# Performance work log

Measured on AMD Instinct MI355X. Metric: run time of the kernel, lower is better.

Reference implementation:

```python
import jax, jax.numpy as jnp
import numpy as np

T, H, I = 8192, 2048, 768  # tokens, hidden_size, intermediate_size

def setup_inputs() -> dict:
    key = jax.random.key(0)
    k1, k2, k3, k4 = jax.random.split(key, 4)
    x = jax.random.normal(k1, (T, H), dtype=jnp.float32)
    # torch nn.Linear weight layout: [out_features, in_features]
    gate_w = jax.random.normal(k2, (I, H), dtype=jnp.float32) * (1.0 / np.sqrt(H))
    up_w = jax.random.normal(k3, (I, H), dtype=jnp.float32) * (1.0 / np.sqrt(H))
    down_w = jax.random.normal(k4, (H, I), dtype=jnp.float32) * (1.0 / np.sqrt(I))
    return {"x": x, "gate_w": gate_w, "up_w": up_w, "down_w": down_w}

def reference(x, gate_w, up_w, down_w):
    # fused SwiGLU MLP: down( silu(x @ gate^T) * (x @ up^T) )
    gate = jnp.einsum('th,ih->ti', x, gate_w)   # [T, I]
    up = jnp.einsum('th,ih->ti', x, up_w)       # [T, I]
    h = jax.nn.silu(gate) * up                   # [T, I]
    out = jnp.einsum('ti,hi->th', h, down_w)     # [T, H]
    return out
```

## Files before the change

### kernel.cpp

```cpp
#include <hip/hip_runtime.h>
#include <hip/hip_bf16.h>
#include <stdint.h>

#define T_DIM 8192
#define H_DIM 2048
#define I_DIM 768

typedef __bf16 bf16_t;
typedef bf16_t bf16x8 __attribute__((ext_vector_type(8)));
typedef bf16_t bf16x4 __attribute__((ext_vector_type(4)));
typedef float  f32x4  __attribute__((ext_vector_type(4)));

__device__ __forceinline__ void async_load16(const void* g, void* s) {
    __builtin_amdgcn_global_load_lds(
        (const __attribute__((address_space(1))) void*)g,
        (__attribute__((address_space(3))) void*)s, 16, 0, 0);
}

__global__ __launch_bounds__(256) void cvt_kernel(
    const float* __restrict__ X, const float* __restrict__ G,
    const float* __restrict__ U, const float* __restrict__ D,
    bf16_t* __restrict__ Xb, bf16_t* __restrict__ Gb,
    bf16_t* __restrict__ Ub, bf16_t* __restrict__ Db)
{
    const size_t N8X = (size_t)T_DIM * H_DIM / 8;
    const size_t N8W = (size_t)I_DIM * H_DIM / 8;
    const size_t total = N8X + 3 * N8W;
    for (size_t i = (size_t)blockIdx.x * blockDim.x + threadIdx.x; i < total;
         i += (size_t)gridDim.x * blockDim.x) {
        const float* s; bf16_t* d; size_t j = i;
        if (j < N8X) { s = X; d = Xb; }
        else {
            j -= N8X;
            if (j < N8W) { s = G; d = Gb; }
            else { j -= N8W;
                if (j < N8W) { s = U; d = Ub; }
                else { j -= N8W; s = D; d = Db; } }
        }
        float4 v0 = ((const float4*)s)[2 * j];
        float4 v1 = ((const float4*)s)[2 * j + 1];
        bf16x8 o;
        o[0] = (bf16_t)v0.x; o[1] = (bf16_t)v0.y; o[2] = (bf16_t)v0.z; o[3] = (bf16_t)v0.w;
        o[4] = (bf16_t)v1.x; o[5] = (bf16_t)v1.y; o[6] = (bf16_t)v1.z; o[7] = (bf16_t)v1.w;
        ((bf16x8*)d)[j] = o;
    }
}

__global__ __launch_bounds__(256) void gateup_kernel(
    const bf16_t* __restrict__ X,
    const bf16_t* __restrict__ Wg,
    const bf16_t* __restrict__ Wu,
    bf16_t* __restrict__ Hbuf)
{
    __shared__ __align__(16) bf16_t sA[128 * 32];
    __shared__ __align__(16) bf16_t sG[64 * 32];
    __shared__ __align__(16) bf16_t sU[64 * 32];

    const int tid   = threadIdx.x;
    const int lane  = tid & 63;
    const int wave  = tid >> 6;
    const int waveM = wave >> 1;
    const int waveN = wave & 1;
    const int quad  = lane >> 4;
    const int lrow  = lane & 15;

    const int blockM = blockIdx.x;
    const int blockN = blockIdx.y;

    f32x4 accG[4][2], accU[4][2];
#pragma unroll
    for (int i = 0; i < 4; i++)
#pragma unroll
        for (int j = 0; j < 2; j++) { accG[i][j] = (f32x4)(0.f); accU[i][j] = (f32x4)(0.f); }

    const int s0 = tid, s1 = tid + 256;
    const int rA0 = s0 >> 2, cA0 = (s0 & 3) * 8;
    const int rA1 = s1 >> 2, cA1 = (s1 & 3) * 8;
    const int rW  = tid >> 2, cW  = (tid & 3) * 8;

    const bf16_t* Ab = X  + (size_t)(blockM * 128) * H_DIM;
    const bf16_t* Gb = Wg + (size_t)(blockN * 64) * H_DIM;
    const bf16_t* Ub = Wu + (size_t)(blockN * 64) * H_DIM;

    for (int k0 = 0; k0 < H_DIM; k0 += 32) {
        async_load16(Ab + (size_t)rA0 * H_DIM + k0 + cA0, &sA[s0 * 8]);
        async_load16(Ab + (size_t)rA1 * H_DIM + k0 + cA1, &sA[s1 * 8]);
        async_load16(Gb + (size_t)rW  * H_DIM + k0 + cW,  &sG[tid * 8]);
        async_load16(Ub + (size_t)rW  * H_DIM + k0 + cW,  &sU[tid * 8]);
        __syncthreads();

        bf16x8 aF[4], gF[2], uF[2];
#pragma unroll
        for (int mi = 0; mi < 4; mi++) {
            int r = waveM * 64 + mi * 16 + lrow;
            aF[mi] = *(const bf16x8*)&sA[r * 32 + quad * 8];
        }
#pragma unroll
        for (int ni = 0; ni < 2; ni++) {
            int r = waveN * 32 + ni * 16 + lrow;
            gF[ni] = *(const bf16x8*)&sG[r * 32 + quad * 8];
            uF[ni] = *(const bf16x8*)&sU[r * 32 + quad * 8];
        }
        __syncthreads();

#pragma unroll
        for (int mi = 0; mi < 4; mi++)
#pragma unroll
            for (int ni = 0; ni < 2; ni++) {
                accG[mi][ni] = __builtin_amdgcn_mfma_f32_16x16x32_bf16(aF[mi], gF[ni], accG[mi][ni], 0, 0, 0);
                accU[mi][ni] = __builtin_amdgcn_mfma_f32_16x16x32_bf16(aF[mi], uF[ni], accU[mi][ni], 0, 0, 0);
            }
    }

#pragma unroll
    for (int mi = 0; mi < 4; mi++) {
#pragma unroll
        for (int ni = 0; ni < 2; ni++) {
#pragma unroll
            for (int r = 0; r < 4; r++) {
                int row = blockM * 128 + waveM * 64 + mi * 16 + quad * 4 + r;
                int col = blockN * 64 + waveN * 32 + ni * 16 + lrow;
                float g = accG[mi][ni][r];
                float u = accU[mi][ni][r];
                float h = (g / (1.f + __expf(-g))) * u;
                Hbuf[(size_t)row * I_DIM + col] = (bf16_t)h;
            }
        }
    }
}

__global__ __launch_bounds__(256, 4) void down_kernel(
    const bf16_t* __restrict__ Hbuf,
    const bf16_t* __restrict__ Wd,
    float* __restrict__ Out)
{
    __shared__ __align__(16) bf16_t sA[128 * 64];
    __shared__ __align__(16) bf16_t sB[128 * 64];

    const int tid   = threadIdx.x;
    const int lane  = tid & 63;
    const int wave  = tid >> 6;
    const int waveM = wave >> 1;
    const int waveN = wave & 1;
    const int quad  = lane >> 4;
    const int lrow  = lane & 15;

    const int blockM = blockIdx.x;
    const int blockN = blockIdx.y;

    f32x4 acc[4][4];
#pragma unroll
    for (int i = 0; i < 4; i++)
#pragma unroll
        for (int j = 0; j < 4; j++) acc[i][j] = (f32x4)(0.f);

    const bf16_t* Ab = Hbuf + (size_t)(blockM * 128) * I_DIM;
    const bf16_t* Bb = Wd   + (size_t)(blockN * 128) * I_DIM;

    int gRow[4], gCol[4];
#pragma unroll
    for (int i = 0; i < 4; i++) {
        int s = tid + 256 * i;
        gRow[i] = s >> 3;
        gCol[i] = ((s & 7) ^ ((s >> 3) & 7)) * 8;
    }

    int aOff[4], bOff[4];
#pragma unroll
    for (int mi = 0; mi < 4; mi++) {
        int r = waveM * 64 + mi * 16 + lrow;
        aOff[mi] = r * 64 + ((quad ^ (r & 7)) * 8);
    }
#pragma unroll
    for (int ni = 0; ni < 4; ni++) {
        int r = waveN * 64 + ni * 16 + lrow;
        bOff[ni] = r * 64 + ((quad ^ (r & 7)) * 8);
    }

    for (int k0 = 0; k0 < I_DIM; k0 += 64) {
#pragma unroll
        for (int i = 0; i < 4; i++) {
            async_load16(Ab + (size_t)gRow[i] * I_DIM + k0 + gCol[i],
                         &sA[(tid + 256 * i) * 8]);
            async_load16(Bb + (size_t)gRow[i] * I_DIM + k0 + gCol[i],
                         &sB[(tid + 256 * i) * 8]);
        }
        __syncthreads();

#pragma unroll
        for (int kk = 0; kk < 2; kk++) {
            const int kx = kk * 32;
            bf16x8 aF[4], bF[4];
#pragma unroll
            for (int mi = 0; mi < 4; mi++)
                aF[mi] = *(const bf16x8*)&sA[aOff[mi] ^ kx];
#pragma unroll
            for (int ni = 0; ni < 4; ni++)
                bF[ni] = *(const bf16x8*)&sB[bOff[ni] ^ kx];
#pragma unroll
            for (int mi = 0; mi < 4; mi++)
#pragma unroll
                for (int ni = 0; ni < 4; ni++)
                    acc[mi][ni] = __builtin_amdgcn_mfma_f32_16x16x32_bf16(aF[mi], bF[ni], acc[mi][ni], 0, 0, 0);
        }
        __syncthreads();
    }

#pragma unroll
    for (int mi = 0; mi < 4; mi++) {
#pragma unroll
        for (int ni = 0; ni < 4; ni++) {
#pragma unroll
            for (int r = 0; r < 4; r++) {
                int row = blockM * 128 + waveM * 64 + mi * 16 + quad * 4 + r;
                int col = blockN * 128 + waveN * 64 + ni * 16 + lrow;
                Out[(size_t)row * H_DIM + col] = acc[mi][ni][r];
            }
        }
    }
}

extern "C" void kernel_launch(void* const* d_in, const int* in_sizes, int n_in,
                              void* d_out, int out_size, void* d_ws, size_t ws_size,
                              hipStream_t stream) {
    const float* x  = (const float*)d_in[0];
    const float* gw = (const float*)d_in[1];
    const float* uw = (const float*)d_in[2];
    const float* dw = (const float*)d_in[3];
    float* out = (float*)d_out;

    bf16_t* xb = (bf16_t*)d_ws;
    bf16_t* gb = xb + (size_t)T_DIM * H_DIM;
    bf16_t* ub = gb + (size_t)I_DIM * H_DIM;
    bf16_t* db = ub + (size_t)I_DIM * H_DIM;
    bf16_t* hb = db + (size_t)I_DIM * H_DIM;

    cvt_kernel<<<2048, 256, 0, stream>>>(x, gw, uw, dw, xb, gb, ub, db);
    gateup_kernel<<<dim3(T_DIM / 128, I_DIM / 64), 256, 0, stream>>>(xb, gb, ub, hb);
    down_kernel<<<dim3(T_DIM / 128, H_DIM / 128), 256, 0, stream>>>(hb, db, out);
}
```

Before: 223.2 us.

## Use 512-thread blocks in gate/up kernel with XOR-swizzled LDS tiles

The gate/up GEMM kernel now runs 8 waves per block instead of 4. Each wave computes a 64x16 slice instead of 64x32, so per-thread accumulators shrink and more waves can hide latency. The LDS fill is spread so each thread issues two async loads, and the LDS layout is XOR-swizzled to cut bank conflicts on fragment reads. The cost is lower MFMA work per wave relative to LDS reads, plus more barrier participants per iteration.

```diff
diff --git a/kernel.cpp b/kernel.cpp
--- a/kernel.cpp
+++ b/kernel.cpp
@@ -46,7 +46,7 @@
     }
 }
 
-__global__ __launch_bounds__(256) void gateup_kernel(
+__global__ __launch_bounds__(512, 8) void gateup_kernel(
     const bf16_t* __restrict__ X,
     const bf16_t* __restrict__ Wg,
     const bf16_t* __restrict__ Wu,
@@ -59,72 +59,66 @@
     const int tid   = threadIdx.x;
     const int lane  = tid & 63;
     const int wave  = tid >> 6;
-    const int waveM = wave >> 1;
-    const int waveN = wave & 1;
+    const int waveM = wave >> 2;
+    const int waveN = wave & 3;
     const int quad  = lane >> 4;
     const int lrow  = lane & 15;
 
     const int blockM = blockIdx.x;
     const int blockN = blockIdx.y;
 
-    f32x4 accG[4][2], accU[4][2];
-#pragma unroll
-    for (int i = 0; i < 4; i++)
-#pragma unroll
-        for (int j = 0; j < 2; j++) { accG[i][j] = (f32x4)(0.f); accU[i][j] = (f32x4)(0.f); }
-
-    const int s0 = tid, s1 = tid + 256;
-    const int rA0 = s0 >> 2, cA0 = (s0 & 3) * 8;
-    const int rA1 = s1 >> 2, cA1 = (s1 & 3) * 8;
-    const int rW  = tid >> 2, cW  = (tid & 3) * 8;
+    f32x4 accG[4], accU[4];
+#pragma unroll
+    for (int i = 0; i < 4; i++) { accG[i] = (f32x4)(0.f); accU[i] = (f32x4)(0.f); }
+
+    const int sa = tid;
+    const int rA = sa >> 2, cA = (((sa & 3) ^ ((rA >> 1) & 3)) * 8);
+    const int sw = tid & 255;
+    const int rW = sw >> 2, cW = (((sw & 3) ^ ((rW >> 1) & 3)) * 8);
 
     const bf16_t* Ab = X  + (size_t)(blockM * 128) * H_DIM;
-    const bf16_t* Gb = Wg + (size_t)(blockN * 64) * H_DIM;
-    const bf16_t* Ub = Wu + (size_t)(blockN * 64) * H_DIM;
+    const bf16_t* Wb = ((tid < 256) ? Wg : Wu) + (size_t)(blockN * 64) * H_DIM;
+    bf16_t* sW = (tid < 256) ? &sG[sw * 8] : &sU[sw * 8];
+
+    int aOff[4];
+#pragma unroll
+    for (int mi = 0; mi < 4; mi++) {
+        int r = waveM * 64 + mi * 16 + lrow;
+        aOff[mi] = r * 32 + ((quad ^ ((r >> 1) & 3)) * 8);
+    }
+    const int rw = waveN * 16 + lrow;
+    const int wOff = rw * 32 + ((quad ^ ((rw >> 1) & 3)) * 8);
 
     for (int k0 = 0; k0 < H_DIM; k0 += 32) {
-        async_load16(Ab + (size_t)rA0 * H_DIM + k0 + cA0, &sA[s0 * 8]);
-        async_load16(Ab + (size_t)rA1 * H_DIM + k0 + cA1, &sA[s1 * 8]);
-        async_load16(Gb + (size_t)rW  * H_DIM + k0 + cW,  &sG[tid * 8]);
-        async_load16(Ub + (size_t)rW  * H_DIM + k0 + cW,  &sU[tid * 8]);
-        __syncthreads();
-
-        bf16x8 aF[4], gF[2], uF[2];
+        async_load16(Ab + (size_t)rA * H_DIM + k0 + cA, &sA[sa * 8]);
+        async_load16(Wb + (size_t)rW * H_DIM + k0 + cW, sW);
+        __syncthreads();
+
+        bf16x8 aF[4], gF, uF;
+#pragma unroll
+        for (int mi = 0; mi < 4; mi++)
+            aF[mi] = *(const bf16x8*)&sA[aOff[mi]];
+        gF = *(const bf16x8*)&sG[wOff];
+        uF = *(const bf16x8*)&sU[wOff];
+        __syncthreads();
+
 #pragma unroll
         for (int mi = 0; mi < 4; mi++) {
-            int r = waveM * 64 + mi * 16 + lrow;
-            aF[mi] = *(const bf16x8*)&sA[r * 32 + quad * 8];
-        }
-#pragma unroll
-        for (int ni = 0; ni < 2; ni++) {
-            int r = waveN * 32 + ni * 16 + lrow;
-            gF[ni] = *(const bf16x8*)&sG[r * 32 + quad * 8];
-            uF[ni] = *(const bf16x8*)&sU[r * 32 + quad * 8];
-        }
-        __syncthreads();
-
-#pragma unroll
-        for (int mi = 0; mi < 4; mi++)
-#pragma unroll
-            for (int ni = 0; ni < 2; ni++) {
-                accG[mi][ni] = __builtin_amdgcn_mfma_f32_16x16x32_bf16(aF[mi], gF[ni], accG[mi][ni], 0, 0, 0);
-                accU[mi][ni] = __builtin_amdgcn_mfma_f32_16x16x32_bf16(aF[mi], uF[ni], accU[mi][ni], 0, 0, 0);
-            }
-    }
-
-#pragma unroll
-    for (int mi = 0; mi < 4; mi++) {
-#pragma unroll
-        for (int ni = 0; ni < 2; ni++) {
-#pragma unroll
-            for (int r = 0; r < 4; r++) {
-                int row = blockM * 128 + waveM * 64 + mi * 16 + quad * 4 + r;
-                int col = blockN * 64 + waveN * 32 + ni * 16 + lrow;
-                float g = accG[mi][ni][r];
-                float u = accU[mi][ni][r];
-                float h = (g / (1.f + __expf(-g))) * u;
-                Hbuf[(size_t)row * I_DIM + col] = (bf16_t)h;
-            }
+            accG[mi] = __builtin_amdgcn_mfma_f32_16x16x32_bf16(aF[mi], gF, accG[mi], 0, 0, 0);
+            accU[mi] = __builtin_amdgcn_mfma_f32_16x16x32_bf16(aF[mi], uF, accU[mi], 0, 0, 0);
+        }
+    }
+
+#pragma unroll
+    for (int mi = 0; mi < 4; mi++) {
+#pragma unroll
+        for (int r = 0; r < 4; r++) {
+            int row = blockM * 128 + waveM * 64 + mi * 16 + quad * 4 + r;
+            int col = blockN * 64 + waveN * 16 + lrow;
+            float g = accG[mi][r];
+            float u = accU[mi][r];
+            float h = (g / (1.f + __expf(-g))) * u;
+            Hbuf[(size_t)row * I_DIM + col] = (bf16_t)h;
         }
     }
 }
@@ -236,6 +230,6 @@
     bf16_t* hb = db + (size_t)I_DIM * H_DIM;
 
     cvt_kernel<<<2048, 256, 0, stream>>>(x, gw, uw, dw, xb, gb, ub, db);
-    gateup_kernel<<<dim3(T_DIM / 128, I_DIM / 64), 256, 0, stream>>>(xb, gb, ub, hb);
+    gateup_kernel<<<dim3(T_DIM / 128, I_DIM / 64), 512, 0, stream>>>(xb, gb, ub, hb);
     down_kernel<<<dim3(T_DIM / 128, H_DIM / 128), 256, 0, stream>>>(hb, db, out);
 }
```

Result: slower. 262.0 us (+17.4%).

## Fuse fp32-to-bf16 conversion of X and gate/up weights into gate-up GEMM

Applied to the files above, without the earlier changes.

Removes the separate conversion pass for X, gate and up weights. The gate/up kernel now loads fp32 tiles into registers, converts them to bf16 and stores them into XOR-swizzled LDS, with precomputed fragment offsets. Only the down weights are still pre-converted, in a smaller kernel. This saves a full write and re-read of the bf16 activation copy. In exchange, global reads are fp32 (twice the bytes for reused tiles) and the async global-to-LDS loads become synchronous register loads, which may expose latency.

```diff
diff --git a/kernel.cpp b/kernel.cpp
--- a/kernel.cpp
+++ b/kernel.cpp
@@ -17,39 +17,29 @@
         (__attribute__((address_space(3))) void*)s, 16, 0, 0);
 }
 
-__global__ __launch_bounds__(256) void cvt_kernel(
-    const float* __restrict__ X, const float* __restrict__ G,
-    const float* __restrict__ U, const float* __restrict__ D,
-    bf16_t* __restrict__ Xb, bf16_t* __restrict__ Gb,
-    bf16_t* __restrict__ Ub, bf16_t* __restrict__ Db)
+__device__ __forceinline__ bf16x8 cvt8(float4 a, float4 b) {
+    bf16x8 o;
+    o[0] = (bf16_t)a.x; o[1] = (bf16_t)a.y; o[2] = (bf16_t)a.z; o[3] = (bf16_t)a.w;
+    o[4] = (bf16_t)b.x; o[5] = (bf16_t)b.y; o[6] = (bf16_t)b.z; o[7] = (bf16_t)b.w;
+    return o;
+}
+
+__global__ __launch_bounds__(256) void cvt_d_kernel(
+    const float* __restrict__ D, bf16_t* __restrict__ Db)
 {
-    const size_t N8X = (size_t)T_DIM * H_DIM / 8;
-    const size_t N8W = (size_t)I_DIM * H_DIM / 8;
-    const size_t total = N8X + 3 * N8W;
-    for (size_t i = (size_t)blockIdx.x * blockDim.x + threadIdx.x; i < total;
-         i += (size_t)gridDim.x * blockDim.x) {
-        const float* s; bf16_t* d; size_t j = i;
-        if (j < N8X) { s = X; d = Xb; }
-        else {
-            j -= N8X;
-            if (j < N8W) { s = G; d = Gb; }
-            else { j -= N8W;
-                if (j < N8W) { s = U; d = Ub; }
-                else { j -= N8W; s = D; d = Db; } }
-        }
-        float4 v0 = ((const float4*)s)[2 * j];
-        float4 v1 = ((const float4*)s)[2 * j + 1];
-        bf16x8 o;
-        o[0] = (bf16_t)v0.x; o[1] = (bf16_t)v0.y; o[2] = (bf16_t)v0.z; o[3] = (bf16_t)v0.w;
-        o[4] = (bf16_t)v1.x; o[5] = (bf16_t)v1.y; o[6] = (bf16_t)v1.z; o[7] = (bf16_t)v1.w;
-        ((bf16x8*)d)[j] = o;
+    const size_t N8 = (size_t)I_DIM * H_DIM / 8;
+    for (size_t j = (size_t)blockIdx.x * blockDim.x + threadIdx.x; j < N8;
+         j += (size_t)gridDim.x * blockDim.x) {
+        float4 v0 = ((const float4*)D)[2 * j];
+        float4 v1 = ((const float4*)D)[2 * j + 1];
+        ((bf16x8*)Db)[j] = cvt8(v0, v1);
     }
 }
 
 __global__ __launch_bounds__(256) void gateup_kernel(
-    const bf16_t* __restrict__ X,
-    const bf16_t* __restrict__ Wg,
-    const bf16_t* __restrict__ Wu,
+    const float* __restrict__ Xf,
+    const float* __restrict__ Wgf,
+    const float* __restrict__ Wuf,
     bf16_t* __restrict__ Hbuf)
 {
     __shared__ __align__(16) bf16_t sA[128 * 32];
@@ -78,30 +68,55 @@
     const int rA1 = s1 >> 2, cA1 = (s1 & 3) * 8;
     const int rW  = tid >> 2, cW  = (tid & 3) * 8;
 
-    const bf16_t* Ab = X  + (size_t)(blockM * 128) * H_DIM;
-    const bf16_t* Gb = Wg + (size_t)(blockN * 64) * H_DIM;
-    const bf16_t* Ub = Wu + (size_t)(blockN * 64) * H_DIM;
+    const int dA0 = rA0 * 32 + (((s0 & 3) ^ ((rA0 >> 1) & 3)) * 8);
+    const int dA1 = rA1 * 32 + (((s1 & 3) ^ ((rA1 >> 1) & 3)) * 8);
+    const int dW  = rW  * 32 + (((tid & 3) ^ ((rW  >> 1) & 3)) * 8);
+
+    const float* Ab0 = Xf  + (size_t)(blockM * 128 + rA0) * H_DIM + cA0;
+    const float* Ab1 = Xf  + (size_t)(blockM * 128 + rA1) * H_DIM + cA1;
+    const float* Gb  = Wgf + (size_t)(blockN * 64  + rW ) * H_DIM + cW;
+    const float* Ub  = Wuf + (size_t)(blockN * 64  + rW ) * H_DIM + cW;
+
+    int aOff[4], wOff[2];
+#pragma unroll
+    for (int mi = 0; mi < 4; mi++) {
+        int r = waveM * 64 + mi * 16 + lrow;
+        aOff[mi] = r * 32 + ((quad ^ ((r >> 1) & 3)) * 8);
+    }
+#pragma unroll
+    for (int ni = 0; ni < 2; ni++) {
+        int r = waveN * 32 + ni * 16 + lrow;
+        wOff[ni] = r * 32 + ((quad ^ ((r >> 1) & 3)) * 8);
+    }
 
     for (int k0 = 0; k0 < H_DIM; k0 += 32) {
-        async_load16(Ab + (size_t)rA0 * H_DIM + k0 + cA0, &sA[s0 * 8]);
-        async_load16(Ab + (size_t)rA1 * H_DIM + k0 + cA1, &sA[s1 * 8]);
-        async_load16(Gb + (size_t)rW  * H_DIM + k0 + cW,  &sG[tid * 8]);
-        async_load16(Ub + (size_t)rW  * H_DIM + k0 + cW,  &sU[tid * 8]);
+        float4 a00 = ((const float4*)(Ab0 + k0))[0];
+        float4 a01 = ((const float4*)(Ab0 + k0))[1];
+        float4 a10 = ((const float4*)(Ab1 + k0))[0];
+        float4 a11 = ((const float4*)(Ab1 + k0))[1];
+        float4 g0  = ((const float4*)(Gb  + k0))[0];
+        float4 g1  = ((const float4*)(Gb  + k0))[1];
+        float4 u0  = ((const float4*)(Ub  + k0))[0];
+        float4 u1  = ((const float4*)(Ub  + k0))[1];
+
+        __syncthreads();
+
+        *(bf16x8*)&sA[dA0] = cvt8(a00, a01);
+        *(bf16x8*)&sA[dA1] = cvt8(a10, a11);
+        *(bf16x8*)&sG[dW]  = cvt8(g0, g1);
+        *(bf16x8*)&sU[dW]  = cvt8(u0, u1);
+
         __syncthreads();
 
         bf16x8 aF[4], gF[2], uF[2];
 #pragma unroll
-        for (int mi = 0; mi < 4; mi++) {
-            int r = waveM * 64 + mi * 16 + lrow;
-            aF[mi] = *(const bf16x8*)&sA[r * 32 + quad * 8];
-        }
+        for (int mi = 0; mi < 4; mi++)
+            aF[mi] = *(const bf16x8*)&sA[aOff[mi]];
 #pragma unroll
         for (int ni = 0; ni < 2; ni++) {
-            int r = waveN * 32 + ni * 16 + lrow;
-            gF[ni] = *(const bf16x8*)&sG[r * 32 + quad * 8];
-            uF[ni] = *(const bf16x8*)&sU[r * 32 + quad * 8];
-        }
-        __syncthreads();
+            gF[ni] = *(const bf16x8*)&sG[wOff[ni]];
+            uF[ni] = *(const bf16x8*)&sU[wOff[ni]];
+        }
 
 #pragma unroll
         for (int mi = 0; mi < 4; mi++)
@@ -229,13 +244,10 @@
     const float* dw = (const float*)d_in[3];
     float* out = (float*)d_out;
 
-    bf16_t* xb = (bf16_t*)d_ws;
-    bf16_t* gb = xb + (size_t)T_DIM * H_DIM;
-    bf16_t* ub = gb + (size_t)I_DIM * H_DIM;
-    bf16_t* db = ub + (size_t)I_DIM * H_DIM;
+    bf16_t* db = (bf16_t*)d_ws;
     bf16_t* hb = db + (size_t)I_DIM * H_DIM;
 
-    cvt_kernel<<<2048, 256, 0, stream>>>(x, gw, uw, dw, xb, gb, ub, db);
-    gateup_kernel<<<dim3(T_DIM / 128, I_DIM / 64), 256, 0, stream>>>(xb, gb, ub, hb);
+    cvt_d_kernel<<<512, 256, 0, stream>>>(dw, db);
+    gateup_kernel<<<dim3(T_DIM / 128, I_DIM / 64), 256, 0, stream>>>(x, gw, uw, hb);
     down_kernel<<<dim3(T_DIM / 128, H_DIM / 128), 256, 0, stream>>>(hb, db, out);
 }
```

New measurement: 236.4 us. 1.06x slower.

## Double-buffer down GEMM with 256x256 tiles and phased MFMA scheduling

Applied to the files above, without the earlier changes.

Rewrites the down-projection kernel to use 512-thread blocks computing 256x256 output tiles, with double-buffered LDS staging of H and the down weights. Async loads for the next K-tiles are issued between MFMA phases, with explicit waitcnt, barriers and priority hints, so that memory traffic overlaps compute. The larger tiles increase data reuse, but they use a large amount of LDS and give a grid of only 256 blocks, which limits occupancy and load balance.

```diff
diff --git a/kernel.cpp b/kernel.cpp
--- a/kernel.cpp
+++ b/kernel.cpp
@@ -15,6 +15,19 @@
     __builtin_amdgcn_global_load_lds(
         (const __attribute__((address_space(1))) void*)g,
         (__attribute__((address_space(3))) void*)s, 16, 0, 0);
+}
+
+__device__ __forceinline__ void phase_barrier() {
+    asm volatile("" ::: "memory");
+    __builtin_amdgcn_s_barrier();
+    asm volatile("" ::: "memory");
+}
+
+__device__ __forceinline__ bf16x8 cvt8(float4 a, float4 b) {
+    bf16x8 o;
+    o[0] = (bf16_t)a.x; o[1] = (bf16_t)a.y; o[2] = (bf16_t)a.z; o[3] = (bf16_t)a.w;
+    o[4] = (bf16_t)b.x; o[5] = (bf16_t)b.y; o[6] = (bf16_t)b.z; o[7] = (bf16_t)b.w;
+    return o;
 }
 
 __global__ __launch_bounds__(256) void cvt_kernel(
@@ -39,10 +52,7 @@
         }
         float4 v0 = ((const float4*)s)[2 * j];
         float4 v1 = ((const float4*)s)[2 * j + 1];
-        bf16x8 o;
-        o[0] = (bf16_t)v0.x; o[1] = (bf16_t)v0.y; o[2] = (bf16_t)v0.z; o[3] = (bf16_t)v0.w;
-        o[4] = (bf16_t)v1.x; o[5] = (bf16_t)v1.y; o[6] = (bf16_t)v1.z; o[7] = (bf16_t)v1.w;
-        ((bf16x8*)d)[j] = o;
+        ((bf16x8*)d)[j] = cvt8(v0, v1);
     }
 }
 
@@ -129,91 +139,126 @@
     }
 }
 
-__global__ __launch_bounds__(256, 4) void down_kernel(
+__global__ __launch_bounds__(512, 2) void down_kernel(
     const bf16_t* __restrict__ Hbuf,
     const bf16_t* __restrict__ Wd,
     float* __restrict__ Out)
 {
-    __shared__ __align__(16) bf16_t sA[128 * 64];
-    __shared__ __align__(16) bf16_t sB[128 * 64];
-
-    const int tid   = threadIdx.x;
-    const int lane  = tid & 63;
-    const int wave  = tid >> 6;
-    const int waveM = wave >> 1;
-    const int waveN = wave & 1;
-    const int quad  = lane >> 4;
-    const int lrow  = lane & 15;
-
-    const int blockM = blockIdx.x;
-    const int blockN = blockIdx.y;
-
-    f32x4 acc[4][4];
-#pragma unroll
-    for (int i = 0; i < 4; i++)
+    __shared__ __align__(16) bf16_t sA[2][256 * 64];
+    __shared__ __align__(16) bf16_t sB[2][256 * 64];
+
+    const int tid  = threadIdx.x;
+    const int lane = tid & 63;
+    const int wave = tid >> 6;
+    const int wm   = wave >> 2;
+    const int wn   = wave & 3;
+    const int quad = lane >> 4;
+    const int lrow = lane & 15;
+
+    const int bm = blockIdx.x;
+    const int bn = blockIdx.y;
+
+    f32x4 acc[8][4];
+#pragma unroll
+    for (int i = 0; i < 8; i++)
 #pragma unroll
         for (int j = 0; j < 4; j++) acc[i][j] = (f32x4)(0.f);
 
-    const bf16_t* Ab = Hbuf + (size_t)(blockM * 128) * I_DIM;
-    const bf16_t* Bb = Wd   + (size_t)(blockN * 128) * I_DIM;
-
-    int gRow[4], gCol[4];
+    int stRow[4], stCol[4];
 #pragma unroll
     for (int i = 0; i < 4; i++) {
-        int s = tid + 256 * i;
-        gRow[i] = s >> 3;
-        gCol[i] = ((s & 7) ^ ((s >> 3) & 7)) * 8;
-    }
-
-    int aOff[4], bOff[4];
-#pragma unroll
-    for (int mi = 0; mi < 4; mi++) {
-        int r = waveM * 64 + mi * 16 + lrow;
+        int s = tid + 512 * i;
+        stRow[i] = s >> 3;
+        stCol[i] = ((s & 7) ^ ((s >> 3) & 7)) * 8;
+    }
+
+    const bf16_t* Ab = Hbuf + (size_t)(bm * 256) * I_DIM;
+    const bf16_t* Bb = Wd   + (size_t)(bn * 256) * I_DIM;
+
+#define STAGE_A(t) do { _Pragma("unroll") \
+    for (int i_ = 0; i_ < 4; i_++) \
+        async_load16(Ab + (size_t)stRow[i_] * I_DIM + (t) * 64 + stCol[i_], \
+                     &sA[(t) & 1][(tid + 512 * i_) * 8]); } while (0)
+#define STAGE_B(t) do { _Pragma("unroll") \
+    for (int i_ = 0; i_ < 4; i_++) \
+        async_load16(Bb + (size_t)stRow[i_] * I_DIM + (t) * 64 + stCol[i_], \
+                     &sB[(t) & 1][(tid + 512 * i_) * 8]); } while (0)
+
+    int aOff[8], bOff[4];
+#pragma unroll
+    for (int mi = 0; mi < 8; mi++) {
+        int r = wm * 128 + mi * 16 + lrow;
         aOff[mi] = r * 64 + ((quad ^ (r & 7)) * 8);
     }
 #pragma unroll
     for (int ni = 0; ni < 4; ni++) {
-        int r = waveN * 64 + ni * 16 + lrow;
+        int r = wn * 64 + ni * 16 + lrow;
         bOff[ni] = r * 64 + ((quad ^ (r & 7)) * 8);
     }
 
-    for (int k0 = 0; k0 < I_DIM; k0 += 64) {
-#pragma unroll
-        for (int i = 0; i < 4; i++) {
-            async_load16(Ab + (size_t)gRow[i] * I_DIM + k0 + gCol[i],
-                         &sA[(tid + 256 * i) * 8]);
-            async_load16(Bb + (size_t)gRow[i] * I_DIM + k0 + gCol[i],
-                         &sB[(tid + 256 * i) * 8]);
-        }
-        __syncthreads();
-
-#pragma unroll
-        for (int kk = 0; kk < 2; kk++) {
-            const int kx = kk * 32;
-            bf16x8 aF[4], bF[4];
-#pragma unroll
-            for (int mi = 0; mi < 4; mi++)
-                aF[mi] = *(const bf16x8*)&sA[aOff[mi] ^ kx];
-#pragma unroll
-            for (int ni = 0; ni < 4; ni++)
-                bF[ni] = *(const bf16x8*)&sB[bOff[ni] ^ kx];
-#pragma unroll
-            for (int mi = 0; mi < 4; mi++)
+    const int nt = I_DIM / 64;
+
+    STAGE_A(0); STAGE_B(0); STAGE_B(1);
+    asm volatile("s_waitcnt vmcnt(4)" ::: "memory");
+    phase_barrier();
+
+    for (int t = 0; t < nt; ++t) {
+        const int p = t & 1;
+        bf16x8 bF[4][2];
+
+#pragma unroll
+        for (int q = 0; q < 4; ++q) {
+            bf16x8 aF[2][2];
+            if (q == 0) {
+#pragma unroll
+                for (int ni = 0; ni < 4; ni++) {
+                    bF[ni][0] = *(const bf16x8*)&sB[p][bOff[ni]];
+                    bF[ni][1] = *(const bf16x8*)&sB[p][bOff[ni] ^ 32];
+                }
+            }
+#pragma unroll
+            for (int j = 0; j < 2; j++) {
+                aF[j][0] = *(const bf16x8*)&sA[p][aOff[2 * q + j]];
+                aF[j][1] = *(const bf16x8*)&sA[p][aOff[2 * q + j] ^ 32];
+            }
+            if (q == 0 && t + 1 < nt) STAGE_A(t + 1);
+            if (q == 1 && t + 2 < nt) STAGE_B(t + 2);
+
+            phase_barrier();
+            asm volatile("s_waitcnt lgkmcnt(0)" ::: "memory");
+            __builtin_amdgcn_sched_barrier(0);
+            __builtin_amdgcn_s_setprio(1);
+#pragma unroll
+            for (int j = 0; j < 2; j++)
 #pragma unroll
                 for (int ni = 0; ni < 4; ni++)
-                    acc[mi][ni] = __builtin_amdgcn_mfma_f32_16x16x32_bf16(aF[mi], bF[ni], acc[mi][ni], 0, 0, 0);
-        }
-        __syncthreads();
-    }
-
-#pragma unroll
-    for (int mi = 0; mi < 4; mi++) {
+#pragma unroll
+                    for (int kk = 0; kk < 2; kk++)
+                        acc[2 * q + j][ni] = __builtin_amdgcn_mfma_f32_16x16x32_bf16(
+                            aF[j][kk], bF[ni][kk], acc[2 * q + j][ni], 0, 0, 0);
+            __builtin_amdgcn_s_setprio(0);
+            if (q < 3) phase_barrier();
+        }
+
+        if (t < nt - 2) {
+            asm volatile("s_waitcnt vmcnt(4)" ::: "memory");
+            phase_barrier();
+        } else if (t == nt - 2) {
+            asm volatile("s_waitcnt vmcnt(0)" ::: "memory");
+            phase_barrier();
+        }
+    }
+#undef STAGE_A
+#undef STAGE_B
+
+#pragma unroll
+    for (int mi = 0; mi < 8; mi++) {
 #pragma unroll
         for (int ni = 0; ni < 4; ni++) {
 #pragma unroll
             for (int r = 0; r < 4; r++) {
-                int row = blockM * 128 + waveM * 64 + mi * 16 + quad * 4 + r;
-                int col = blockN * 128 + waveN * 64 + ni * 16 + lrow;
+                int row = bm * 256 + wm * 128 + mi * 16 + quad * 4 + r;
+                int col = bn * 256 + wn * 64 + ni * 16 + lrow;
                 Out[(size_t)row * H_DIM + col] = acc[mi][ni][r];
             }
         }
@@ -237,5 +282,5 @@
 
     cvt_kernel<<<2048, 256, 0, stream>>>(x, gw, uw, dw, xb, gb, ub, db);
     gateup_kernel<<<dim3(T_DIM / 128, I_DIM / 64), 256, 0, stream>>>(xb, gb, ub, hb);
-    down_kernel<<<dim3(T_DIM / 128, H_DIM / 128), 256, 0, stream>>>(hb, db, out);
-}
+    down_kernel<<<dim3(T_DIM / 256, H_DIM / 256), 512, 0, stream>>>(hb, db, out);
+}
```

Measured after the change: 221.5 us. No clear change (-0.7%).
